# Optimization experiments

Hardware: AMD Instinct MI355X
Metric: run time of the kernel (lower is better)

The kernel has to match this reference:

```python
import math
import jax, jax.numpy as jnp
import numpy as np

B, C, H, W = 16, 512, 32, 32
NUM_HEADS = 4
GROUPS = 32
EPS = 1e-5


def setup_inputs() -> dict:
    key = jax.random.key(0)
    ks = jax.random.split(key, 3)
    x = jax.random.normal(ks[0], (B, C, H, W), dtype=jnp.float32)
    # conv weights: kaiming-ish scale for 1x1 convs (fan_in = C)
    qkv_w = jax.random.normal(ks[1], (3 * C, C), dtype=jnp.float32) * (1.0 / math.sqrt(C))
    proj_w = jax.random.normal(ks[2], (C, C), dtype=jnp.float32) * (1.0 / math.sqrt(C))
    return {
        "x": x,
        "norm_w": jnp.ones((C,), jnp.float32),
        "norm_b": jnp.zeros((C,), jnp.float32),
        "qkv_w": qkv_w,
        "qkv_b": jnp.zeros((3 * C,), jnp.float32),
        "proj_w": proj_w,
        "proj_b": jnp.zeros((C,), jnp.float32),
    }


def group_norm(x, w, b):
    bN, c, h, wd = x.shape
    xg = x.reshape(bN, GROUPS, c // GROUPS, h, wd)
    mean = xg.mean(axis=(2, 3, 4), keepdims=True)
    var = xg.var(axis=(2, 3, 4), keepdims=True)
    xg = (xg - mean) * jax.lax.rsqrt(var + EPS)
    x = xg.reshape(bN, c, h, wd)
    return x * w[None, :, None, None] + b[None, :, None, None]


def conv1x1(x, w, b):
    # x: (b,c,h,w), w: (out,in), b: (out,)
    return jnp.einsum('bchw,oc->bohw', x, w) + b[None, :, None, None]


def reference(x, norm_w, norm_b, qkv_w, qkv_b, proj_w, proj_b):
    b, c, h, w = x.shape
    hd = c // NUM_HEADS  # head dim
    n = h * w            # tokens
    qkv = conv1x1(group_norm(x, norm_w, norm_b), qkv_w, qkv_b)
    q, k, v = jnp.split(qkv, 3, axis=1)
    # (b, heads, hd, n)
    q = q.reshape(b, NUM_HEADS, hd, n)
    k = k.reshape(b, NUM_HEADS, hd, n)
    v = v.reshape(b, NUM_HEADS, hd, n)
    # attn: (b, heads, n, n)
    attn = jnp.einsum('bhdn,bhdm->bhnm', q, k) / math.sqrt(hd)
    attn = jax.nn.softmax(attn, axis=-1)
    # out: (b, heads, n, hd) -> (b, c, h, w)
    out = jnp.einsum('bhnm,bhdm->bhnd', attn, v)
    out = out.transpose(0, 1, 3, 2).reshape(b, c, h, w)
    return x + conv1x1(out, proj_w, proj_b)
```

## Files before the change

### kernel.cpp

```cpp
#include <hip/hip_runtime.h>
#include <stdint.h>

#define DEV __device__ __forceinline__

typedef __attribute__((ext_vector_type(4))) float f32x4;
typedef __attribute__((ext_vector_type(16))) float f32x16;
typedef __attribute__((ext_vector_type(8))) short s16x8;
typedef __attribute__((ext_vector_type(8))) __bf16 bf16x8;

constexpr int kB = 16, kC = 512, kN = 1024;
constexpr int kO = 1536;
constexpr int kG = 32, kCPG = 16;
constexpr float kEps = 1e-5f;
constexpr float kQS = 0.08838834764831845f * 1.44269504088896f;

#if __has_builtin(__builtin_amdgcn_exp2f)
#define EXP2(x) __builtin_amdgcn_exp2f(x)
#else
#define EXP2(x) exp2f(x)
#endif

DEV unsigned short f2bf(float f) {
  union { float f; uint32_t u; } cv; cv.f = f;
  uint32_t u = cv.u;
  return (unsigned short)((u + 0x7FFFu + ((u >> 16) & 1u)) >> 16);
}

DEV unsigned short bfbits(float f) {
  __bf16 h = (__bf16)f;
  return __builtin_bit_cast(unsigned short, h);
}

DEV bf16x8 asbf(s16x8 v) { return __builtin_bit_cast(bf16x8, v); }

DEV uint32_t cvtpk(float a, float b) {
  uint32_t w;
  asm("v_cvt_pk_bf16_f32 %0, %1, %2" : "=v"(w) : "v"(a), "v"(b));
  return w;
}

DEV void gl_lds16(const void* g, void* l) {
  __builtin_amdgcn_global_load_lds(
      (const __attribute__((address_space(1))) uint32_t*)g,
      (__attribute__((address_space(3))) uint32_t*)l, 16, 0, 0);
}

__global__ __launch_bounds__(256) void k_wconv2(const float* __restrict__ qw,
                                                const float* __restrict__ pw,
                                                unsigned short* __restrict__ dq,
                                                unsigned short* __restrict__ dp) {
  const int nq = 1536 * 512 / 4, np = 512 * 512 / 4;
  int i = blockIdx.x * 256 + threadIdx.x;
  const float* src;
  unsigned short* dst;
  int j;
  if (i < nq) { src = qw; dst = dq; j = i; }
  else { j = i - nq; if (j >= np) return; src = pw; dst = dp; }
  f32x4 v = ((const f32x4*)src)[j];
  unsigned short o[4];
  o[0] = f2bf(v[0]); o[1] = f2bf(v[1]); o[2] = f2bf(v[2]); o[3] = f2bf(v[3]);
  ((uint2*)dst)[j] = *(uint2*)o;
}

__global__ __launch_bounds__(256) void k_gnstats(const float* __restrict__ x,
                                                 float* __restrict__ meanp,
                                                 float* __restrict__ rstdp) {
  int bg = blockIdx.x;
  const f32x4* p4 = (const f32x4*)(x + (size_t)bg * (kCPG * kN));
  float s = 0.f, s2 = 0.f;
  for (int i = threadIdx.x; i < (kCPG * kN / 4); i += 256) {
    f32x4 v = p4[i];
    s += v[0] + v[1] + v[2] + v[3];
    s2 += v[0] * v[0] + v[1] * v[1] + v[2] * v[2] + v[3] * v[3];
  }
#pragma unroll
  for (int m = 32; m >= 1; m >>= 1) { s += __shfl_xor(s, m); s2 += __shfl_xor(s2, m); }
  __shared__ float rb[8];
  int lane = threadIdx.x & 63, wid = threadIdx.x >> 6;
  if (lane == 0) { rb[wid * 2] = s; rb[wid * 2 + 1] = s2; }
  __syncthreads();
  if (threadIdx.x == 0) {
    float S = rb[0] + rb[2] + rb[4] + rb[6];
    float S2 = rb[1] + rb[3] + rb[5] + rb[7];
    float mu = S * (1.f / 16384.f);
    float var = S2 * (1.f / 16384.f) - mu * mu;
    meanp[bg] = mu;
    rstdp[bg] = rsqrtf(var + kEps);
  }
}

__global__ __launch_bounds__(256) void k_gnapply(const float* __restrict__ x,
                                                 const float* __restrict__ gw,
                                                 const float* __restrict__ gb,
                                                 const float* __restrict__ meanp,
                                                 const float* __restrict__ rstdp,
                                                 unsigned short* __restrict__ xt) {
  int bid = blockIdx.x;
  int b = bid >> 7;
  int ct = (bid >> 4) & 7;
  int nt = bid & 15;
  int c0 = ct * 64, n0 = nt * 64;
  __shared__ float tile[64][65];
  int t = threadIdx.x;
#pragma unroll
  for (int pass = 0; pass < 4; ++pass) {
    int r = pass * 16 + (t >> 4);
    int col = (t & 15) << 2;
    int c = c0 + r;
    f32x4 v = *(const f32x4*)(x + ((size_t)b * kC + c) * kN + n0 + col);
    int g = b * kG + (c >> 4);
    float rs = rstdp[g];
    float a = rs * gw[c];
    float bb = gb[c] - meanp[g] * a;
    tile[r][col + 0] = v[0] * a + bb;
    tile[r][col + 1] = v[1] * a + bb;
    tile[r][col + 2] = v[2] * a + bb;
    tile[r][col + 3] = v[3] * a + bb;
  }
  __syncthreads();
#pragma unroll
  for (int pass = 0; pass < 2; ++pass) {
    int nr = pass * 32 + (t >> 3);
    int cb = (t & 7) << 3;
    unsigned short o[8];
#pragma unroll
    for (int j = 0; j < 8; ++j) o[j] = f2bf(tile[cb + j][nr]);
    *(uint4*)(xt + ((size_t)b * kN + n0 + nr) * kC + c0 + cb) = *(uint4*)o;
  }
}

template <int MODE>
__global__ __launch_bounds__(256, 3) void k_gemm(const unsigned short* __restrict__ act,
                                                 const unsigned short* __restrict__ wb,
                                                 const float* __restrict__ bias,
                                                 unsigned short* __restrict__ qkT,
                                                 unsigned short* __restrict__ vbuf,
                                                 const float* __restrict__ xres,
                                                 float* __restrict__ outp) {
  int b = blockIdx.y;
  int nt = blockIdx.x & 7, ot = blockIdx.x >> 3;
  int n0 = nt << 7, o0 = ot << 7;
  int t = threadIdx.x, lane = t & 63, wid = t >> 6;
  int wr = wid >> 1, wc = wid & 1;
  __shared__ __align__(16) char smem[49152];
  f32x4 acc[4][4];
  const f32x4 zf = {0.f, 0.f, 0.f, 0.f};
#pragma unroll
  for (int i = 0; i < 4; ++i)
#pragma unroll
    for (int j = 0; j < 4; ++j) acc[i][j] = zf;
  const size_t rowb = (size_t)b * kN;

  auto stage = [&](int buf, int kt2) {
    const int k0 = kt2 << 5;
    char* dA = smem + buf * 8192;
    char* dB = smem + 24576 + buf * 8192;
#pragma unroll
    for (int p = 0; p < 2; ++p) {
      const int id = p * 256 + t;
      const int row = id >> 2, cp = id & 3;
      const int cl = cp ^ ((row >> 1) & 3);
      gl_lds16(act + (rowb + n0 + row) * (size_t)kC + k0 + cl * 8, dA + id * 16);
      gl_lds16(wb + (size_t)(o0 + row) * kC + k0 + cl * 8, dB + id * 16);
    }
  };

  stage(0, 0);
  stage(1, 1);
  int cur = 0, stg = 2;
#pragma unroll 1
  for (int kt = 0; kt < 16; ++kt) {
    if (kt < 15) {
      asm volatile("s_waitcnt vmcnt(4)" ::: "memory");
    } else {
      asm volatile("s_waitcnt vmcnt(0)" ::: "memory");
    }
    __builtin_amdgcn_s_barrier();
    if (kt < 14) stage(stg, kt + 2);
    const char* pA = smem + cur * 8192;
    const char* pB = smem + 24576 + cur * 8192;
    s16x8 af[4], bfr[4];
    const int c = lane >> 4;
#pragma unroll
    for (int i = 0; i < 4; ++i) {
      const int rA = wr * 64 + i * 16 + (lane & 15);
      af[i] = *(const s16x8*)(pA + rA * 64 + ((c ^ ((rA >> 1) & 3)) << 4));
      const int rB = wc * 64 + i * 16 + (lane & 15);
      bfr[i] = *(const s16x8*)(pB + rB * 64 + ((c ^ ((rB >> 1) & 3)) << 4));
    }
    __builtin_amdgcn_s_setprio(1);
#pragma unroll
    for (int i = 0; i < 4; ++i)
#pragma unroll
      for (int j = 0; j < 4; ++j)
        acc[i][j] = __builtin_amdgcn_mfma_f32_16x16x32_bf16(asbf(af[i]), asbf(bfr[j]),
                                                            acc[i][j], 0, 0, 0);
    __builtin_amdgcn_s_setprio(0);
    cur = (cur == 2) ? 0 : cur + 1;
    stg = (stg == 2) ? 0 : stg + 1;
  }

  if (MODE == 0) {
    if (o0 < 1024) {
      __syncthreads();
      const float sc = (o0 < 512) ? kQS : 1.0f;
      unsigned short* tile = (unsigned short*)smem;
#pragma unroll
      for (int j = 0; j < 4; ++j) {
        const int o = wc * 64 + j * 16 + (lane & 15);
        const float bs = bias[o0 + o];
#pragma unroll
        for (int i = 0; i < 4; ++i)
#pragma unroll
          for (int r = 0; r < 4; ++r) {
            const int n = wr * 64 + i * 16 + ((lane >> 4) << 2) + r;
            tile[n * 136 + o] = f2bf((acc[i][j][r] + bs) * sc);
          }
      }
      __syncthreads();
#pragma unroll
      for (int it = 0; it < 8; ++it) {
        const int n = it * 16 + (t >> 4);
        const int c8 = t & 15;
        *(uint4*)(qkT + (rowb + n0 + n) * (size_t)kO + o0 + c8 * 8) =
            *(const uint4*)(tile + n * 136 + c8 * 8);
      }
    } else {
#pragma unroll
      for (int j = 0; j < 4; ++j) {
        const int o = o0 + wc * 64 + j * 16 + (lane & 15);
        const float bs = bias[o];
#pragma unroll
        for (int i = 0; i < 4; ++i) {
          const int nb = n0 + wr * 64 + ((lane >> 4) << 2) + i * 16;
          unsigned short pk[4];
#pragma unroll
          for (int r = 0; r < 4; ++r) pk[r] = f2bf(acc[i][j][r] + bs);
          *(uint2*)(vbuf + ((size_t)b * 512 + (o - 1024)) * kN + nb) = *(uint2*)pk;
        }
      }
    }
  } else {
    const int baseN = n0 + wr * 64 + ((lane >> 4) << 2);
#pragma unroll
    for (int j = 0; j < 4; ++j) {
      const int o = o0 + wc * 64 + j * 16 + (lane & 15);
      const float bs = bias[o];
#pragma unroll
      for (int i = 0; i < 4; ++i) {
        const int nb = baseN + i * 16;
        const size_t oo = ((size_t)b * kC + o) * kN + nb;
        const f32x4 xv = *(const f32x4*)(xres + oo);
        f32x4 ov;
        ov[0] = acc[i][j][0] + bs + xv[0];
        ov[1] = acc[i][j][1] + bs + xv[1];
        ov[2] = acc[i][j][2] + bs + xv[2];
        ov[3] = acc[i][j][3] + bs + xv[3];
        *(f32x4*)(outp + oo) = ov;
      }
    }
  }
}

__global__ __launch_bounds__(256, 3) void k_attn(const unsigned short* __restrict__ qkT,
                                                 const unsigned short* __restrict__ vbuf,
                                                 unsigned short* __restrict__ aoT) {
  const int bh = blockIdx.x, qt = blockIdx.y;
  const int b = bh >> 2, h = bh & 3;
  const int t = threadIdx.x, lane = t & 63, wid = t >> 6;
  const int l31 = lane & 31, hi = lane >> 5;
  __shared__ unsigned short sK[2][64 * 128];
  __shared__ unsigned short sV[128 * 64];
  __shared__ float sL[4][32];
  const int qrow0 = qt * 128 + wid * 32;
  s16x8 qf[8];
#pragma unroll
  for (int kk = 0; kk < 8; ++kk)
    qf[kk] = *(const s16x8*)(qkT + ((size_t)b * kN + qrow0 + l31) * kO + h * 128 +
                             kk * 16 + hi * 8);
  f32x16 oc[4];
#pragma unroll
  for (int df = 0; df < 4; ++df)
#pragma unroll
    for (int r = 0; r < 16; ++r) oc[df][r] = 0.f;
  float lpart = 0.f;

  auto stageK = [&](int buf, int m0) {
#pragma unroll
    for (int p = 0; p < 4; ++p) {
      const int id = p * 256 + t;
      const int row = id >> 4, cp = id & 15, cl = cp ^ (row & 7);
      gl_lds16(qkT + ((size_t)b * kN + m0 + row) * kO + 512 + h * 128 + cl * 8,
               (char*)sK[buf] + (p * 256 + wid * 64) * 16);
    }
  };
  auto stageV = [&](int m0) {
#pragma unroll
    for (int p = 0; p < 4; ++p) {
      const int id = p * 256 + t;
      const int row = id >> 3, cp = id & 7, cl = cp ^ (row & 7);
      gl_lds16(vbuf + ((size_t)b * 512 + h * 128 + row) * kN + m0 + cl * 8,
               (char*)sV + (p * 256 + wid * 64) * 16);
    }
  };
  auto qkhalf = [&](int cur, int rbase, float& ps, uint32_t paw[2][4]) {
    float p[16];
    {
      f32x16 sa;
#pragma unroll
      for (int r = 0; r < 16; ++r) sa[r] = 0.f;
      __builtin_amdgcn_s_setprio(1);
#pragma unroll
      for (int kk = 0; kk < 8; ++kk) {
        const int c0 = kk * 2 + hi;
        const int r0 = rbase + l31;
        s16x8 kf = *(const s16x8*)((const char*)sK[cur] + r0 * 256 + ((c0 ^ (r0 & 7)) << 4));
        sa = __builtin_amdgcn_mfma_f32_32x32x16_bf16(asbf(kf), asbf(qf[kk]), sa, 0, 0, 0);
      }
      __builtin_amdgcn_s_setprio(0);
#pragma unroll
      for (int r = 0; r < 16; ++r) { p[r] = EXP2(sa[r]); ps += p[r]; }
    }
#pragma unroll
    for (int half = 0; half < 2; ++half) {
      const int base = half * 8;
      uint32_t a0 = cvtpk(p[base + 0], p[base + 1]);
      uint32_t b0 = cvtpk(p[base + 4], p[base + 5]);
      asm volatile("v_permlane32_swap_b32 %0, %1" : "+v"(a0), "+v"(b0));
      uint32_t a1 = cvtpk(p[base + 2], p[base + 3]);
      uint32_t b1 = cvtpk(p[base + 6], p[base + 7]);
      asm volatile("v_permlane32_swap_b32 %0, %1" : "+v"(a1), "+v"(b1));
      paw[half][0] = a0; paw[half][1] = a1; paw[half][2] = b0; paw[half][3] = b1;
    }
  };
  auto pv2 = [&](int ksbase, const uint32_t paw[2][4]) {
    __builtin_amdgcn_s_setprio(1);
#pragma unroll
    for (int k2 = 0; k2 < 2; ++k2) {
      union { uint32_t w[4]; s16x8 v; } pa;
      pa.w[0] = paw[k2][0]; pa.w[1] = paw[k2][1]; pa.w[2] = paw[k2][2]; pa.w[3] = paw[k2][3];
      const int cv = (ksbase + k2) * 2 + hi;
#pragma unroll
      for (int df = 0; df < 4; ++df) {
        const int rv = df * 32 + l31;
        s16x8 vf = *(const s16x8*)((const char*)sV + rv * 128 + ((cv ^ (rv & 7)) << 4));
        oc[df] = __builtin_amdgcn_mfma_f32_32x32x16_bf16(asbf(pa.v), asbf(vf), oc[df], 0, 0, 0);
      }
    }
    __builtin_amdgcn_s_setprio(0);
  };

  stageK(0, 0);
#pragma unroll 1
  for (int mt = 0; mt < 16; ++mt) {
    const int cur = mt & 1;
    asm volatile("s_waitcnt vmcnt(0)" ::: "memory");
    __builtin_amdgcn_s_barrier();
    stageV(mt * 64);
    if (mt < 15) stageK(cur ^ 1, (mt + 1) * 64);
    float ps = 0.f;
    uint32_t paw[2][4];
    qkhalf(cur, 0, ps, paw);
    if (mt < 15) {
      asm volatile("s_waitcnt vmcnt(4)" ::: "memory");
    } else {
      asm volatile("s_waitcnt vmcnt(0)" ::: "memory");
    }
    __builtin_amdgcn_s_barrier();
    pv2(0, paw);
    qkhalf(cur, 32, ps, paw);
    pv2(2, paw);
    lpart += ps;
  }
  lpart += __shfl_xor(lpart, 32);
  if (hi == 0) sL[wid][l31] = lpart;
  float inv[16];
#pragma unroll
  for (int r = 0; r < 16; ++r) {
    const int crow = (r & 3) + 8 * (r >> 2) + 4 * hi;
    inv[r] = 1.f / sL[wid][crow];
  }
#pragma unroll
  for (int df = 0; df < 4; ++df) {
    const int d = df * 32 + l31;
#pragma unroll
    for (int r = 0; r < 16; ++r) {
      const int n = qrow0 + (r & 3) + 8 * (r >> 2) + 4 * hi;
      aoT[((size_t)b * kN + n) * kC + h * 128 + d] = bfbits(oc[df][r] * inv[r]);
    }
  }
}

extern "C" void kernel_launch(void* const* d_in, const int* in_sizes, int n_in,
                              void* d_out, int out_size, void* d_ws, size_t ws_size,
                              hipStream_t stream) {
  const float* x = (const float*)d_in[0];
  const float* norm_w = (const float*)d_in[1];
  const float* norm_b = (const float*)d_in[2];
  const float* qkv_w = (const float*)d_in[3];
  const float* qkv_b = (const float*)d_in[4];
  const float* proj_w = (const float*)d_in[5];
  const float* proj_b = (const float*)d_in[6];
  float* out = (float*)d_out;
  char* ws = (char*)d_ws;
  const size_t OFF_MEAN = 0;
  const size_t OFF_RSTD = 2048;
  const size_t OFF_WQ = 4096;
  const size_t OFF_WP = OFF_WQ + (size_t)1536 * 512 * 2;
  const size_t OFF_XT = OFF_WP + (size_t)512 * 512 * 2;
  const size_t OFF_QKT = OFF_XT + (size_t)16 * 1024 * 512 * 2;
  const size_t OFF_V = OFF_QKT + (size_t)16 * 1024 * 1536 * 2;
  const size_t NEED = OFF_V + (size_t)16 * 512 * 1024 * 2;
  if (ws_size < NEED) return;
  float* meanp = (float*)(ws + OFF_MEAN);
  float* rstdp = (float*)(ws + OFF_RSTD);
  unsigned short* wq = (unsigned short*)(ws + OFF_WQ);
  unsigned short* wp = (unsigned short*)(ws + OFF_WP);
  unsigned short* xt = (unsigned short*)(ws + OFF_XT);
  unsigned short* qkT = (unsigned short*)(ws + OFF_QKT);
  unsigned short* vb = (unsigned short*)(ws + OFF_V);
  unsigned short* aoT = xt;

  k_wconv2<<<1024, 256, 0, stream>>>(qkv_w, proj_w, wq, wp);
  k_gnstats<<<512, 256, 0, stream>>>(x, meanp, rstdp);
  k_gnapply<<<2048, 256, 0, stream>>>(x, norm_w, norm_b, meanp, rstdp, xt);
  k_gemm<0><<<dim3(96, 16), 256, 0, stream>>>(xt, wq, qkv_b, qkT, vb, nullptr, nullptr);
  k_attn<<<dim3(64, 8), 256, 0, stream>>>(qkT, vb, aoT);
  k_gemm<1><<<dim3(32, 16), 256, 0, stream>>>(aoT, wp, proj_b, nullptr, nullptr, x, out);
}
```

Measured before the change: 120.7 us.

## Widen attention blocks to 8 waves and double-buffer V with K

The attention kernel now runs 512 threads per block covering 256 query rows, so each staged K/V tile is shared by twice as many waves and the grid halves. V is double-buffered alongside K and prefetched one tile ahead, which removes the mid-iteration wait and barrier. The QK^T dot product is split into two independent MFMA accumulator chains to shorten dependency stalls. The cost is more LDS per block (double V) and more registers from the extra accumulator, which may lower occupancy, and the grid of 256 blocks may underfill the CUs.

```diff
diff --git a/kernel.cpp b/kernel.cpp
--- a/kernel.cpp
+++ b/kernel.cpp
@@ -262,7 +262,7 @@
   }
 }
 
-__global__ __launch_bounds__(256, 3) void k_attn(const unsigned short* __restrict__ qkT,
+__global__ __launch_bounds__(512, 2) void k_attn(const unsigned short* __restrict__ qkT,
                                                  const unsigned short* __restrict__ vbuf,
                                                  unsigned short* __restrict__ aoT) {
   const int bh = blockIdx.x, qt = blockIdx.y;
@@ -270,9 +270,9 @@
   const int t = threadIdx.x, lane = t & 63, wid = t >> 6;
   const int l31 = lane & 31, hi = lane >> 5;
   __shared__ unsigned short sK[2][64 * 128];
-  __shared__ unsigned short sV[128 * 64];
-  __shared__ float sL[4][32];
-  const int qrow0 = qt * 128 + wid * 32;
+  __shared__ unsigned short sV[2][128 * 64];
+  __shared__ float sL[8][32];
+  const int qrow0 = qt * 256 + wid * 32;
   s16x8 qf[8];
 #pragma unroll
   for (int kk = 0; kk < 8; ++kk)
@@ -287,39 +287,41 @@
 
   auto stageK = [&](int buf, int m0) {
 #pragma unroll
-    for (int p = 0; p < 4; ++p) {
-      const int id = p * 256 + t;
+    for (int p = 0; p < 2; ++p) {
+      const int id = p * 512 + t;
       const int row = id >> 4, cp = id & 15, cl = cp ^ (row & 7);
       gl_lds16(qkT + ((size_t)b * kN + m0 + row) * kO + 512 + h * 128 + cl * 8,
-               (char*)sK[buf] + (p * 256 + wid * 64) * 16);
+               (char*)sK[buf] + (p * 512 + wid * 64) * 16);
     }
   };
-  auto stageV = [&](int m0) {
-#pragma unroll
-    for (int p = 0; p < 4; ++p) {
-      const int id = p * 256 + t;
+  auto stageV = [&](int buf, int m0) {
+#pragma unroll
+    for (int p = 0; p < 2; ++p) {
+      const int id = p * 512 + t;
       const int row = id >> 3, cp = id & 7, cl = cp ^ (row & 7);
       gl_lds16(vbuf + ((size_t)b * 512 + h * 128 + row) * kN + m0 + cl * 8,
-               (char*)sV + (p * 256 + wid * 64) * 16);
+               (char*)sV[buf] + (p * 512 + wid * 64) * 16);
     }
   };
   auto qkhalf = [&](int cur, int rbase, float& ps, uint32_t paw[2][4]) {
     float p[16];
     {
-      f32x16 sa;
-#pragma unroll
-      for (int r = 0; r < 16; ++r) sa[r] = 0.f;
+      f32x16 sa, sb;
+#pragma unroll
+      for (int r = 0; r < 16; ++r) { sa[r] = 0.f; sb[r] = 0.f; }
+      const int r0 = rbase + l31;
       __builtin_amdgcn_s_setprio(1);
 #pragma unroll
-      for (int kk = 0; kk < 8; ++kk) {
-        const int c0 = kk * 2 + hi;
-        const int r0 = rbase + l31;
-        s16x8 kf = *(const s16x8*)((const char*)sK[cur] + r0 * 256 + ((c0 ^ (r0 & 7)) << 4));
-        sa = __builtin_amdgcn_mfma_f32_32x32x16_bf16(asbf(kf), asbf(qf[kk]), sa, 0, 0, 0);
+      for (int kk = 0; kk < 4; ++kk) {
+        const int ca = kk * 2 + hi, cb2 = (kk + 4) * 2 + hi;
+        s16x8 kfa = *(const s16x8*)((const char*)sK[cur] + r0 * 256 + ((ca ^ (r0 & 7)) << 4));
+        s16x8 kfb = *(const s16x8*)((const char*)sK[cur] + r0 * 256 + ((cb2 ^ (r0 & 7)) << 4));
+        sa = __builtin_amdgcn_mfma_f32_32x32x16_bf16(asbf(kfa), asbf(qf[kk]), sa, 0, 0, 0);
+        sb = __builtin_amdgcn_mfma_f32_32x32x16_bf16(asbf(kfb), asbf(qf[kk + 4]), sb, 0, 0, 0);
       }
       __builtin_amdgcn_s_setprio(0);
 #pragma unroll
-      for (int r = 0; r < 16; ++r) { p[r] = EXP2(sa[r]); ps += p[r]; }
+      for (int r = 0; r < 16; ++r) { p[r] = EXP2(sa[r] + sb[r]); ps += p[r]; }
     }
 #pragma unroll
     for (int half = 0; half < 2; ++half) {
@@ -333,7 +335,7 @@
       paw[half][0] = a0; paw[half][1] = a1; paw[half][2] = b0; paw[half][3] = b1;
     }
   };
-  auto pv2 = [&](int ksbase, const uint32_t paw[2][4]) {
+  auto pv2 = [&](int cur, int ksbase, const uint32_t paw[2][4]) {
     __builtin_amdgcn_s_setprio(1);
 #pragma unroll
     for (int k2 = 0; k2 < 2; ++k2) {
@@ -343,7 +345,7 @@
 #pragma unroll
       for (int df = 0; df < 4; ++df) {
         const int rv = df * 32 + l31;
-        s16x8 vf = *(const s16x8*)((const char*)sV + rv * 128 + ((cv ^ (rv & 7)) << 4));
+        s16x8 vf = *(const s16x8*)((const char*)sV[cur] + rv * 128 + ((cv ^ (rv & 7)) << 4));
         oc[df] = __builtin_amdgcn_mfma_f32_32x32x16_bf16(asbf(pa.v), asbf(vf), oc[df], 0, 0, 0);
       }
     }
@@ -351,29 +353,27 @@
   };
 
   stageK(0, 0);
+  stageV(0, 0);
 #pragma unroll 1
   for (int mt = 0; mt < 16; ++mt) {
     const int cur = mt & 1;
     asm volatile("s_waitcnt vmcnt(0)" ::: "memory");
     __builtin_amdgcn_s_barrier();
-    stageV(mt * 64);
-    if (mt < 15) stageK(cur ^ 1, (mt + 1) * 64);
+    if (mt < 15) {
+      stageV(cur ^ 1, (mt + 1) * 64);
+      stageK(cur ^ 1, (mt + 1) * 64);
+    }
     float ps = 0.f;
     uint32_t paw[2][4];
     qkhalf(cur, 0, ps, paw);
-    if (mt < 15) {
-      asm volatile("s_waitcnt vmcnt(4)" ::: "memory");
-    } else {
-      asm volatile("s_waitcnt vmcnt(0)" ::: "memory");
-    }
-    __builtin_amdgcn_s_barrier();
-    pv2(0, paw);
+    pv2(cur, 0, paw);
     qkhalf(cur, 32, ps, paw);
-    pv2(2, paw);
+    pv2(cur, 2, paw);
     lpart += ps;
   }
   lpart += __shfl_xor(lpart, 32);
   if (hi == 0) sL[wid][l31] = lpart;
+  __builtin_amdgcn_s_barrier();
   float inv[16];
 #pragma unroll
   for (int r = 0; r < 16; ++r) {
@@ -425,6 +425,6 @@
   k_gnstats<<<512, 256, 0, stream>>>(x, meanp, rstdp);
   k_gnapply<<<2048, 256, 0, stream>>>(x, norm_w, norm_b, meanp, rstdp, xt);
   k_gemm<0><<<dim3(96, 16), 256, 0, stream>>>(xt, wq, qkv_b, qkT, vb, nullptr, nullptr);
-  k_attn<<<dim3(64, 8), 256, 0, stream>>>(qkT, vb, aoT);
+  k_attn<<<dim3(64, 4), 512, 0, stream>>>(qkT, vb, aoT);
   k_gemm<1><<<dim3(32, 16), 256, 0, stream>>>(aoT, wp, proj_b, nullptr, nullptr, x, out);
 }
```

Result: no change. 122.1 us (+1.1%).
